# Kernel optimization log

Measured on AMD Instinct MI355X. Metric: run time of the kernel, lower is better.

## Reference

```python
import jax, jax.numpy as jnp
import numpy as np

T, N, D = 8, 50000, 128
H, M, E = 128, 64, 800000
TW = 10  # temporal conv kernel width


def setup_inputs() -> dict:
    key = jax.random.key(0)
    ks = jax.random.split(key, 16)
    s_d, s_2h, s_m, s_hm = D ** -0.5, (2 * H) ** -0.5, M ** -0.5, (H + M) ** -0.5
    return {
        "node_features": jax.random.normal(ks[0], (T, N, D), jnp.float32),
        "edge_index": jax.random.randint(ks[1], (2, E), 0, N, dtype=jnp.int64),
        # spatial dense [D -> H]
        "W_sp": jax.random.normal(ks[2], (D, H), jnp.float32) * s_d,
        "b_sp": jnp.zeros((H,), jnp.float32),
        # memory projection dense [2H -> M] (inline Dense, modeled shared)
        "W_mp": jax.random.normal(ks[3], (2 * H, M), jnp.float32) * s_2h,
        "b_mp": jnp.zeros((M,), jnp.float32),
        # flax GRUCell: input denses (ir,iz,in) with bias; hidden denses (hr,hz) no bias, hn with bias
        "Wi": jax.random.normal(ks[4], (M, 3 * M), jnp.float32) * s_m,
        "bi": jnp.zeros((3 * M,), jnp.float32),
        "Wh": jax.random.normal(ks[5], (M, 3 * M), jnp.float32) * s_m,
        "bhn": jnp.zeros((M,), jnp.float32),
        # output projection [H+M -> H]
        "W_out": jax.random.normal(ks[6], (H + M, H), jnp.float32) * s_hm,
        "b_out": jnp.zeros((H,), jnp.float32),
        # temporal conv kernel [TW, in=1, out=H] + bias [H] (only channel 0 is used)
        "conv_k": jax.random.normal(ks[7], (TW, 1, H), jnp.float32) * (TW ** -0.5),
        "conv_b": jnp.zeros((H,), jnp.float32),
    }


def _forward(node_features, edge_index, W_sp, b_sp, W_mp, b_mp, Wi, bi, Wh, bhn, W_out, b_out, conv_k, conv_b):
    t, n, _ = node_features.shape
    m = Wi.shape[0]
    src, tgt = edge_index[0], edge_index[1]

    def step(h, x_t):
        s = jax.nn.relu(x_t @ W_sp + b_sp)                       # [N,H]
        msg = jnp.zeros_like(s).at[tgt].add(s[src])               # scatter-add message passing
        mi = jnp.concatenate([s, msg], axis=-1) @ W_mp + b_mp     # [N,M]
        # flax GRUCell
        gi = mi @ Wi + bi                                         # [N,3M]
        gh = h @ Wh                                               # [N,3M] (no bias on hr/hz)
        i_r, i_z, i_n = jnp.split(gi, 3, axis=-1)
        h_r, h_z, h_n = jnp.split(gh, 3, axis=-1)
        r = jax.nn.sigmoid(i_r + h_r)
        z = jax.nn.sigmoid(i_z + h_z)
        nn_ = jnp.tanh(i_n + r * (h_n + bhn))
        h_new = (1.0 - z) * nn_ + z * h
        out = jnp.concatenate([s, h_new], axis=-1) @ W_out + b_out  # [N,H]
        return h_new, out

    h0 = jnp.zeros((n, m), node_features.dtype)
    h_final, outs = jax.lax.scan(step, h0, node_features)         # outs: [T,N,H]

    temporal = jnp.transpose(outs, (1, 0, 2))                     # [N,T,H]
    # flax Conv on [N,T,H,1]: batch=(N,T), spatial=H, in_ch=1; [...,0] keeps out channel 0
    x = temporal.reshape(n * t, -1, 1)                            # [N*T, H, 1]
    k0 = conv_k[:, :, :1]                                         # [TW,1,1]
    y = jax.lax.conv_general_dilated(x, k0, window_strides=(1,), padding="SAME",
                                     dimension_numbers=("NWC", "WIO", "NWC"))
    y = y[..., 0] + conv_b[0]                                     # [N*T, H]
    temporal_out = y.reshape(n, t, -1)                            # [N,T,H]
    final = temporal_out[:, -1, :]                                # [N,H]
    return final, h_final


def reference(node_features, edge_index, W_sp, b_sp, W_mp, b_mp, Wi, bi, Wh, bhn, W_out, b_out, conv_k, conv_b):
    return _forward(node_features, edge_index, W_sp, b_sp, W_mp, b_mp, Wi, bi, Wh, bhn, W_out, b_out, conv_k, conv_b)
```

## Files before the change

kernel.cpp:

```cpp
#include <hip/hip_runtime.h>

#define TT 8
#define NN 50000
#define DD 128
#define HH 128
#define MM 64
#define EE 800000
#define NBLK 196

typedef __attribute__((ext_vector_type(8))) short short8v;
typedef __attribute__((ext_vector_type(4))) float f32x4;

__device__ __forceinline__ short bf16rn(float v) {
    unsigned u = __builtin_bit_cast(unsigned, v);
    unsigned r = (u + 0x7fffu + ((u >> 16) & 1u)) >> 16;
    return (short)r;
}
__device__ __forceinline__ float bf16tof(short h) {
    unsigned u = ((unsigned)(unsigned short)h) << 16;
    return __builtin_bit_cast(float, u);
}
__device__ __forceinline__ void bsplit(float v, short& h, short& l) {
    h = bf16rn(v);
    l = bf16rn(v - bf16tof(h));
}
__device__ __forceinline__ f32x4 mfma16(short8v a, short8v b, f32x4 c) {
    return __builtin_amdgcn_mfma_f32_16x16x32_bf16(a, b, c, 0, 0, 0);
}

__global__ __launch_bounds__(256) void kConvEdges(const int* __restrict__ eraw,
                                                  int* __restrict__ src,
                                                  int* __restrict__ tgt,
                                                  int* __restrict__ deg) {
    bool is64 = true;
#pragma unroll
    for (int i = 0; i < 8; ++i)
        if (eraw[2 * i + 1] != 0) is64 = false;
    int i = blockIdx.x * blockDim.x + threadIdx.x;
    if (i < EE) {
        int s, t;
        if (is64) {
            const long long* e64 = (const long long*)eraw;
            s = (int)e64[i];
            t = (int)e64[EE + i];
        } else {
            s = eraw[i];
            t = eraw[EE + i];
        }
        s = min(max(s, 0), NN - 1);
        t = min(max(t, 0), NN - 1);
        src[i] = s;
        tgt[i] = t;
        atomicAdd(&deg[t], 1);
    }
}

__global__ __launch_bounds__(256) void kScanA(const int* __restrict__ deg,
                                              int* __restrict__ itmp,
                                              int* __restrict__ bsum) {
    __shared__ int sm[256];
    int gid = blockIdx.x * 256 + threadIdx.x;
    int v = (gid < NN) ? deg[gid] : 0;
    sm[threadIdx.x] = v;
    __syncthreads();
    for (int off = 1; off < 256; off <<= 1) {
        int add = (threadIdx.x >= off) ? sm[threadIdx.x - off] : 0;
        __syncthreads();
        sm[threadIdx.x] += add;
        __syncthreads();
    }
    itmp[gid] = sm[threadIdx.x];
    if (threadIdx.x == 255) bsum[blockIdx.x] = sm[255];
}

__global__ __launch_bounds__(256) void kScanB(const int* __restrict__ bsum,
                                              int* __restrict__ boffs) {
    __shared__ int sm[256];
    int v = (threadIdx.x < NBLK) ? bsum[threadIdx.x] : 0;
    sm[threadIdx.x] = v;
    __syncthreads();
    for (int off = 1; off < 256; off <<= 1) {
        int add = (threadIdx.x >= off) ? sm[threadIdx.x - off] : 0;
        __syncthreads();
        sm[threadIdx.x] += add;
        __syncthreads();
    }
    if (threadIdx.x < NBLK)
        boffs[threadIdx.x] = (threadIdx.x == 0) ? 0 : sm[threadIdx.x - 1];
}

__global__ __launch_bounds__(256) void kScanC(const int* __restrict__ itmp,
                                              const int* __restrict__ boffs,
                                              int* __restrict__ rowptr) {
    int gid = blockIdx.x * 256 + threadIdx.x;
    if (gid < NN) rowptr[gid + 1] = itmp[gid] + boffs[blockIdx.x];
    if (gid == 0) rowptr[0] = 0;
}

__global__ __launch_bounds__(256) void kFill(const int* __restrict__ src,
                                             const int* __restrict__ tgt,
                                             const int* __restrict__ rowptr,
                                             int* __restrict__ cursor,
                                             int* __restrict__ csr_src) {
    int e = blockIdx.x * blockDim.x + threadIdx.x;
    if (e < EE) {
        int t = tgt[e];
        int p = atomicAdd(&cursor[t], 1);
        csr_src[rowptr[t] + p] = src[e];
    }
}

__global__ __launch_bounds__(256) void kPrep(const float* __restrict__ Wsp,
                                             const float* __restrict__ Wmp,
                                             const float* __restrict__ bmp,
                                             const float* __restrict__ Wi,
                                             const float* __restrict__ bi,
                                             const float* __restrict__ Wh,
                                             const float* __restrict__ bhn,
                                             short* __restrict__ Bp1,
                                             short* __restrict__ Bp2,
                                             short* __restrict__ Bp3,
                                             float* __restrict__ bias_aq,
                                             float* __restrict__ bias_g) {
    const int gid = blockIdx.x * 256 + threadIdx.x;
    const int gstride = gridDim.x * 256;

    for (int i = gid; i < 8 * 4 * 512; i += gstride) {
        int e = i & 7, lanei = (i >> 3) & 63, kt = (i >> 9) & 3, nt = i >> 11;
        int k = kt * 32 + (lanei >> 4) * 8 + e;
        int col = nt * 16 + (lanei & 15);
        float v = Wsp[k * 128 + col];
        short h, l;
        bsplit(v, h, l);
        Bp1[((nt * 4 + kt) * 2 + 0) * 512 + lanei * 8 + e] = h;
        Bp1[((nt * 4 + kt) * 2 + 1) * 512 + lanei * 8 + e] = l;
    }
    for (int i = gid; i < 8 * 4 * 512; i += gstride) {
        int e = i & 7, lanei = (i >> 3) & 63, kt = (i >> 9) & 3, nt = i >> 11;
        int k = kt * 32 + (lanei >> 4) * 8 + e;
        int col = nt * 16 + (lanei & 15);
        float v = (col < 64) ? Wmp[k * 64 + col] : Wmp[(128 + k) * 64 + (col - 64)];
        short h, l;
        bsplit(v, h, l);
        Bp2[((nt * 4 + kt) * 2 + 0) * 512 + lanei * 8 + e] = h;
        Bp2[((nt * 4 + kt) * 2 + 1) * 512 + lanei * 8 + e] = l;
    }
    for (int i = gid; i < 16 * 4 * 512; i += gstride) {
        int e = i & 7, lanei = (i >> 3) & 63, kt = (i >> 9) & 3, nt = i >> 11;
        int k = kt * 32 + (lanei >> 4) * 8 + e;
        int col = nt * 16 + (lanei & 15);
        float v;
        if (k < 64) {
            v = (col < 192) ? Wi[k * 192 + col] : 0.f;
        } else {
            int kk = k - 64;
            if (col < 128)      v = Wh[kk * 192 + col];
            else if (col < 192) v = 0.f;
            else                v = Wh[kk * 192 + (col - 64)];
        }
        short h, l;
        bsplit(v, h, l);
        Bp3[((nt * 4 + kt) * 2 + 0) * 512 + lanei * 8 + e] = h;
        Bp3[((nt * 4 + kt) * 2 + 1) * 512 + lanei * 8 + e] = l;
    }
    if (gid < 128) bias_aq[gid] = (gid < 64) ? bmp[gid] : 0.f;
    if (gid < 256) bias_g[gid] = (gid < 192) ? bi[gid] : bhn[gid - 192];
}

__global__ __launch_bounds__(256) void kGemm12(const float* __restrict__ A,
                                               const short* __restrict__ Bp,
                                               const float* __restrict__ bias,
                                               float* __restrict__ C,
                                               int relu) {
    const int tid = threadIdx.x, lane = tid & 63, w = tid >> 6;
    const int rowBase = blockIdx.x * 64 + (w & 1) * 32;
    const int colBase = (w >> 1) * 64;

    short8v ah[2][4], al[2][4];
#pragma unroll
    for (int mt = 0; mt < 2; ++mt) {
        int row = min(rowBase + mt * 16 + (lane & 15), NN - 1);
        const float* ar = A + (size_t)row * 128 + (lane >> 4) * 8;
#pragma unroll
        for (int kt = 0; kt < 4; ++kt) {
            float4 x0 = *(const float4*)(ar + kt * 32);
            float4 x1 = *(const float4*)(ar + kt * 32 + 4);
            float xs[8] = {x0.x, x0.y, x0.z, x0.w, x1.x, x1.y, x1.z, x1.w};
#pragma unroll
            for (int e = 0; e < 8; ++e) {
                short h, l;
                bsplit(xs[e], h, l);
                ah[mt][kt][e] = h;
                al[mt][kt][e] = l;
            }
        }
    }

    f32x4 acc[2][4];
#pragma unroll
    for (int mt = 0; mt < 2; ++mt)
#pragma unroll
        for (int nt = 0; nt < 4; ++nt) acc[mt][nt] = (f32x4)0.f;

#pragma unroll
    for (int nt = 0; nt < 4; ++nt) {
        const int ntg = (colBase >> 4) + nt;
#pragma unroll
        for (int kt = 0; kt < 4; ++kt) {
            short8v bh = *(const short8v*)&Bp[((ntg * 4 + kt) * 2 + 0) * 512 + lane * 8];
            short8v bl = *(const short8v*)&Bp[((ntg * 4 + kt) * 2 + 1) * 512 + lane * 8];
#pragma unroll
            for (int mt = 0; mt < 2; ++mt) {
                acc[mt][nt] = mfma16(ah[mt][kt], bh, acc[mt][nt]);
                acc[mt][nt] = mfma16(ah[mt][kt], bl, acc[mt][nt]);
                acc[mt][nt] = mfma16(al[mt][kt], bh, acc[mt][nt]);
            }
        }
    }

#pragma unroll
    for (int mt = 0; mt < 2; ++mt)
#pragma unroll
        for (int nt = 0; nt < 4; ++nt) {
            int col = colBase + nt * 16 + (lane & 15);
            float bb = bias[col];
            int r0 = rowBase + mt * 16 + (lane >> 4) * 4;
#pragma unroll
            for (int r = 0; r < 4; ++r) {
                int row = r0 + r;
                if (row < NN) {
                    float v = acc[mt][nt][r] + bb;
                    if (relu) v = fmaxf(v, 0.f);
                    C[(size_t)row * 128 + col] = v;
                }
            }
        }
}

__global__ __launch_bounds__(256) void kGemm3(float* __restrict__ mih,
                                              const short* __restrict__ Bp,
                                              const float* __restrict__ bias_g) {
    __shared__ float gT[256][36];
    const int tid = threadIdx.x, lane = tid & 63, w = tid >> 6;
    const int rowBase = blockIdx.x * 32;
    const int colBase = w * 64;

    short8v ah[2][4], al[2][4];
#pragma unroll
    for (int mt = 0; mt < 2; ++mt) {
        int row = min(rowBase + mt * 16 + (lane & 15), NN - 1);
        const float* ar = mih + (size_t)row * 128 + (lane >> 4) * 8;
#pragma unroll
        for (int kt = 0; kt < 4; ++kt) {
            float4 x0 = *(const float4*)(ar + kt * 32);
            float4 x1 = *(const float4*)(ar + kt * 32 + 4);
            float xs[8] = {x0.x, x0.y, x0.z, x0.w, x1.x, x1.y, x1.z, x1.w};
#pragma unroll
            for (int e = 0; e < 8; ++e) {
                short h, l;
                bsplit(xs[e], h, l);
                ah[mt][kt][e] = h;
                al[mt][kt][e] = l;
            }
        }
    }

    f32x4 acc[2][4];
#pragma unroll
    for (int mt = 0; mt < 2; ++mt)
#pragma unroll
        for (int nt = 0; nt < 4; ++nt) acc[mt][nt] = (f32x4)0.f;

#pragma unroll
    for (int nt = 0; nt < 4; ++nt) {
        const int ntg = (colBase >> 4) + nt;
#pragma unroll
        for (int kt = 0; kt < 4; ++kt) {
            short8v bh = *(const short8v*)&Bp[((ntg * 4 + kt) * 2 + 0) * 512 + lane * 8];
            short8v bl = *(const short8v*)&Bp[((ntg * 4 + kt) * 2 + 1) * 512 + lane * 8];
#pragma unroll
            for (int mt = 0; mt < 2; ++mt) {
                acc[mt][nt] = mfma16(ah[mt][kt], bh, acc[mt][nt]);
                acc[mt][nt] = mfma16(ah[mt][kt], bl, acc[mt][nt]);
                acc[mt][nt] = mfma16(al[mt][kt], bh, acc[mt][nt]);
            }
        }
    }

#pragma unroll
    for (int mt = 0; mt < 2; ++mt)
#pragma unroll
        for (int nt = 0; nt < 4; ++nt) {
            int col = colBase + nt * 16 + (lane & 15);
            int r0 = mt * 16 + (lane >> 4) * 4;
            f32x4 v = acc[mt][nt] + bias_g[col];
            *(f32x4*)&gT[col][r0] = v;
        }
    __syncthreads();

#pragma unroll
    for (int i = 0; i < 8; ++i) {
        int idx = i * 256 + tid;
        int row = idx & 31, c = idx >> 5;
        int node = rowBase + row;
        if (node >= NN) continue;
        float xr = gT[c][row];
        float xz = gT[c + 64][row];
        float xni = gT[c + 128][row];
        float xnh = gT[c + 192][row];
        float* hp = &mih[(size_t)node * 128 + 64 + c];
        float hv = *hp;
        float r = 1.f / (1.f + __expf(-xr));
        float z = 1.f / (1.f + __expf(-xz));
        float xn = xni + r * xnh;
        float e2 = __expf(2.f * xn);
        float nn = 1.f - 2.f / (e2 + 1.f);
        *hp = (1.f - z) * nn + z * hv;
    }
}

__global__ __launch_bounds__(256) void kGather(const float* __restrict__ aq,
                                               const int* __restrict__ rowptr,
                                               const int* __restrict__ csr_src,
                                               float* __restrict__ mih) {
    const int lane = threadIdx.x & 63;
    const int w = (blockIdx.x * blockDim.x + threadIdx.x) >> 6;
    if (w >= NN) return;
    const int beg = rowptr[w];
    const int end = rowptr[w + 1];
    float acc0 = 0.f, acc1 = 0.f;
    int i = beg;
    for (; i + 1 < end; i += 2) {
        int s0 = csr_src[i];
        int s1 = csr_src[i + 1];
        acc0 += aq[(size_t)s0 * 128 + 64 + lane];
        acc1 += aq[(size_t)s1 * 128 + 64 + lane];
    }
    if (i < end) acc0 += aq[(size_t)csr_src[i] * 128 + 64 + lane];
    mih[(size_t)w * 128 + lane] = acc0 + acc1 + aq[(size_t)w * 128 + lane];
}

__global__ __launch_bounds__(128) void kD(const float* __restrict__ s_buf,
                                          const float* __restrict__ mih,
                                          const float* __restrict__ Wout,
                                          const float* __restrict__ bout,
                                          const float* __restrict__ convk,
                                          const float* __restrict__ convb,
                                          float* __restrict__ out) {
    __shared__ float ss[4][HH];
    __shared__ float hs[4][MM];
    __shared__ float os[4][HH];
    const int j = threadIdx.x;
    const int base = blockIdx.x * 4;

#pragma unroll
    for (int n = 0; n < 4; ++n)
        ss[n][j] = s_buf[(size_t)(base + n) * HH + j];
    for (int idx = j; idx < 4 * MM; idx += 128) {
        int n = idx >> 6, c = idx & 63;
        hs[n][c] = mih[(size_t)(base + n) * 128 + 64 + c];
    }
    __syncthreads();

    float acc[4];
    const float bj = bout[j];
#pragma unroll
    for (int n = 0; n < 4; ++n) acc[n] = bj;
#pragma unroll 4
    for (int k = 0; k < HH; ++k) {
        float w = Wout[k * HH + j];
#pragma unroll
        for (int n = 0; n < 4; ++n) acc[n] = fmaf(ss[n][k], w, acc[n]);
    }
#pragma unroll 4
    for (int k = 0; k < MM; ++k) {
        float w = Wout[(HH + k) * HH + j];
#pragma unroll
        for (int n = 0; n < 4; ++n) acc[n] = fmaf(hs[n][k], w, acc[n]);
    }
#pragma unroll
    for (int n = 0; n < 4; ++n) os[n][j] = acc[n];
    __syncthreads();

    float ck[10];
#pragma unroll
    for (int i = 0; i < 10; ++i) ck[i] = convk[i * HH];
    const float cb = convb[0];
#pragma unroll
    for (int n = 0; n < 4; ++n) {
        float y = cb;
#pragma unroll
        for (int i = 0; i < 10; ++i) {
            int p = j - 4 + i;
            float xv = (p >= 0 && p < HH) ? os[n][p] : 0.f;
            y = fmaf(xv, ck[i], y);
        }
        out[(size_t)(base + n) * HH + j] = y;
    }
    for (int idx = j; idx < 4 * MM; idx += 128) {
        int n = idx >> 6, c = idx & 63;
        out[(size_t)NN * HH + (size_t)(base + n) * MM + c] = hs[n][c];
    }
}

extern "C" void kernel_launch(void* const* d_in, const int* in_sizes, int n_in,
                              void* d_out, int out_size, void* d_ws, size_t ws_size,
                              hipStream_t stream) {
    const float* X    = (const float*)d_in[0];
    const int*   eraw = (const int*)d_in[1];
    const float* Wsp  = (const float*)d_in[2];
    const float* bsp  = (const float*)d_in[3];
    const float* Wmp  = (const float*)d_in[4];
    const float* bmp  = (const float*)d_in[5];
    const float* Wi   = (const float*)d_in[6];
    const float* bi   = (const float*)d_in[7];
    const float* Wh   = (const float*)d_in[8];
    const float* bhn  = (const float*)d_in[9];
    const float* Wout = (const float*)d_in[10];
    const float* bout = (const float*)d_in[11];
    const float* ck   = (const float*)d_in[12];
    const float* cb   = (const float*)d_in[13];
    float* out = (float*)d_out;

    float* ws = (float*)d_ws;
    float* s_buf  = ws;
    float* aq     = s_buf + (size_t)NN * 128;
    float* mih    = aq + (size_t)NN * 128;
    float* bias_aq= mih + (size_t)NN * 128;
    float* bias_g = bias_aq + 128;
    short* Bp1    = (short*)(bias_g + 256);
    short* Bp2    = Bp1 + 8 * 4 * 2 * 512;
    short* Bp3    = Bp2 + 8 * 4 * 2 * 512;
    int*   src     = (int*)(Bp3 + 16 * 4 * 2 * 512);
    int*   tgt     = src + EE;
    int*   csr_src = tgt + EE;
    int*   deg     = csr_src + EE;
    int*   rowptr  = deg + NN;
    int*   cursor  = rowptr + NN + 1;
    int*   itmp    = cursor + NN;
    int*   bsum    = itmp + NBLK * 256;
    int*   boffs   = bsum + 256;

    hipMemsetAsync(mih, 0, (size_t)NN * 128 * sizeof(float), stream);
    hipMemsetAsync(deg, 0, NN * sizeof(int), stream);
    hipMemsetAsync(cursor, 0, NN * sizeof(int), stream);

    kConvEdges<<<(EE + 255) / 256, 256, 0, stream>>>(eraw, src, tgt, deg);
    kScanA<<<NBLK, 256, 0, stream>>>(deg, itmp, bsum);
    kScanB<<<1, 256, 0, stream>>>(bsum, boffs);
    kScanC<<<NBLK, 256, 0, stream>>>(itmp, boffs, rowptr);
    kFill<<<(EE + 255) / 256, 256, 0, stream>>>(src, tgt, rowptr, cursor, csr_src);
    kPrep<<<64, 256, 0, stream>>>(Wsp, Wmp, bmp, Wi, bi, Wh, bhn,
                                  Bp1, Bp2, Bp3, bias_aq, bias_g);

    const int gx12 = (NN + 63) / 64;
    const int gx3  = (NN + 31) / 32;
    for (int t = 0; t < TT; ++t) {
        kGemm12<<<gx12, 256, 0, stream>>>(X + (size_t)t * NN * DD, Bp1, bsp, s_buf, 1);
        kGemm12<<<gx12, 256, 0, stream>>>(s_buf, Bp2, bias_aq, aq, 0);
        kGather<<<(NN * 64 + 255) / 256, 256, 0, stream>>>(aq, rowptr, csr_src, mih);
        kGemm3<<<gx3, 256, 0, stream>>>(mih, Bp3, bias_g);
    }
    kD<<<NN / 4, 128, 0, stream>>>(s_buf, mih, Wout, bout, ck, cb, out);
}
```

Baseline: 1.493 ms.

## Hoist feedforward GEMMs out of time loop and fuse into one batched kernel

The two non-recurrent GEMMs (spatial dense and the memory projection split into a/q halves) are computed for all T timesteps in a single fused kernel. The intermediate s stays in shared memory as packed hi/lo bf16 pairs, and only the last timestep's s is written out. The gathered neighbor projection q is stored as bf16 to halve gather traffic. The GRU input/state buffer is now kept as packed bf16 hi/lo words, so the per-element split no longer runs on load. This removes per-step launches and the round trip of s and aq through global memory, but adds larger a/q workspaces and reduces the precision of the message path and of the stored hidden state.

```diff
diff --git a/kernel.cpp b/kernel.cpp
--- a/kernel.cpp
+++ b/kernel.cpp
@@ -11,18 +11,28 @@
 typedef __attribute__((ext_vector_type(8))) short short8v;
 typedef __attribute__((ext_vector_type(4))) float f32x4;
 
-__device__ __forceinline__ short bf16rn(float v) {
+__device__ __forceinline__ unsigned bf16rn_bits(float v) {
     unsigned u = __builtin_bit_cast(unsigned, v);
-    unsigned r = (u + 0x7fffu + ((u >> 16) & 1u)) >> 16;
-    return (short)r;
-}
-__device__ __forceinline__ float bf16tof(short h) {
-    unsigned u = ((unsigned)(unsigned short)h) << 16;
-    return __builtin_bit_cast(float, u);
+    return (u + 0x7fffu + ((u >> 16) & 1u)) >> 16;
+}
+__device__ __forceinline__ short bf16rn(float v) { return (short)bf16rn_bits(v); }
+__device__ __forceinline__ float bf16tof_bits(unsigned hb16) {
+    return __builtin_bit_cast(float, hb16 << 16);
 }
 __device__ __forceinline__ void bsplit(float v, short& h, short& l) {
     h = bf16rn(v);
-    l = bf16rn(v - bf16tof(h));
+    l = bf16rn(v - bf16tof_bits((unsigned)(unsigned short)h));
+}
+__device__ __forceinline__ unsigned packsplit(float v) {
+    unsigned u = __builtin_bit_cast(unsigned, v);
+    unsigned hb = u & 0xFFFF0000u;
+    float lo = v - __builtin_bit_cast(float, hb);
+    return hb | (bf16rn_bits(lo) & 0xFFFFu);
+}
+__device__ __forceinline__ float unpack_val(unsigned p) {
+    float hi = __builtin_bit_cast(float, p & 0xFFFF0000u);
+    float lo = __builtin_bit_cast(float, p << 16);
+    return hi + lo;
 }
 __device__ __forceinline__ f32x4 mfma16(short8v a, short8v b, f32x4 c) {
     return __builtin_amdgcn_mfma_f32_16x16x32_bf16(a, b, c, 0, 0, 0);
@@ -112,7 +122,6 @@
 
 __global__ __launch_bounds__(256) void kPrep(const float* __restrict__ Wsp,
                                              const float* __restrict__ Wmp,
-                                             const float* __restrict__ bmp,
                                              const float* __restrict__ Wi,
                                              const float* __restrict__ bi,
                                              const float* __restrict__ Wh,
@@ -120,7 +129,6 @@
                                              short* __restrict__ Bp1,
                                              short* __restrict__ Bp2,
                                              short* __restrict__ Bp3,
-                                             float* __restrict__ bias_aq,
                                              float* __restrict__ bias_g) {
     const int gid = blockIdx.x * 256 + threadIdx.x;
     const int gstride = gridDim.x * 256;
@@ -163,24 +171,28 @@
         Bp3[((nt * 4 + kt) * 2 + 0) * 512 + lanei * 8 + e] = h;
         Bp3[((nt * 4 + kt) * 2 + 1) * 512 + lanei * 8 + e] = l;
     }
-    if (gid < 128) bias_aq[gid] = (gid < 64) ? bmp[gid] : 0.f;
     if (gid < 256) bias_g[gid] = (gid < 192) ? bi[gid] : bhn[gid - 192];
 }
 
-__global__ __launch_bounds__(256) void kGemm12(const float* __restrict__ A,
-                                               const short* __restrict__ Bp,
-                                               const float* __restrict__ bias,
-                                               float* __restrict__ C,
-                                               int relu) {
+__global__ __launch_bounds__(256) void kFF(const float* __restrict__ X,
+                                           const short* __restrict__ Bp1,
+                                           const float* __restrict__ bsp,
+                                           const short* __restrict__ Bp2,
+                                           const float* __restrict__ bmp,
+                                           float* __restrict__ a_all,
+                                           unsigned short* __restrict__ qb_all,
+                                           float* __restrict__ s_buf) {
+    __shared__ unsigned sPk[64][132];
     const int tid = threadIdx.x, lane = tid & 63, w = tid >> 6;
-    const int rowBase = blockIdx.x * 64 + (w & 1) * 32;
+    const size_t rowBlk = (size_t)blockIdx.x * 64;
+    const int rhalf = (w & 1) * 32;
     const int colBase = (w >> 1) * 64;
 
     short8v ah[2][4], al[2][4];
 #pragma unroll
     for (int mt = 0; mt < 2; ++mt) {
-        int row = min(rowBase + mt * 16 + (lane & 15), NN - 1);
-        const float* ar = A + (size_t)row * 128 + (lane >> 4) * 8;
+        size_t row = rowBlk + rhalf + mt * 16 + (lane & 15);
+        const float* ar = X + row * 128 + (lane >> 4) * 8;
 #pragma unroll
         for (int kt = 0; kt < 4; ++kt) {
             float4 x0 = *(const float4*)(ar + kt * 32);
@@ -207,8 +219,8 @@
         const int ntg = (colBase >> 4) + nt;
 #pragma unroll
         for (int kt = 0; kt < 4; ++kt) {
-            short8v bh = *(const short8v*)&Bp[((ntg * 4 + kt) * 2 + 0) * 512 + lane * 8];
-            short8v bl = *(const short8v*)&Bp[((ntg * 4 + kt) * 2 + 1) * 512 + lane * 8];
+            short8v bh = *(const short8v*)&Bp1[((ntg * 4 + kt) * 2 + 0) * 512 + lane * 8];
+            short8v bl = *(const short8v*)&Bp1[((ntg * 4 + kt) * 2 + 1) * 512 + lane * 8];
 #pragma unroll
             for (int mt = 0; mt < 2; ++mt) {
                 acc[mt][nt] = mfma16(ah[mt][kt], bh, acc[mt][nt]);
@@ -223,49 +235,36 @@
 #pragma unroll
         for (int nt = 0; nt < 4; ++nt) {
             int col = colBase + nt * 16 + (lane & 15);
-            float bb = bias[col];
-            int r0 = rowBase + mt * 16 + (lane >> 4) * 4;
+            float b = bsp[col];
+            int lr0 = rhalf + mt * 16 + (lane >> 4) * 4;
 #pragma unroll
             for (int r = 0; r < 4; ++r) {
-                int row = r0 + r;
-                if (row < NN) {
-                    float v = acc[mt][nt][r] + bb;
-                    if (relu) v = fmaxf(v, 0.f);
-                    C[(size_t)row * 128 + col] = v;
-                }
-            }
-        }
-}
-
-__global__ __launch_bounds__(256) void kGemm3(float* __restrict__ mih,
-                                              const short* __restrict__ Bp,
-                                              const float* __restrict__ bias_g) {
-    __shared__ float gT[256][36];
-    const int tid = threadIdx.x, lane = tid & 63, w = tid >> 6;
-    const int rowBase = blockIdx.x * 32;
-    const int colBase = w * 64;
-
-    short8v ah[2][4], al[2][4];
+                float sv = fmaxf(acc[mt][nt][r] + b, 0.f);
+                sPk[lr0 + r][col] = packsplit(sv);
+                size_t row = rowBlk + lr0 + r;
+                if (row >= (size_t)(TT - 1) * NN)
+                    s_buf[(row - (size_t)(TT - 1) * NN) * 128 + col] = sv;
+            }
+        }
+    __syncthreads();
+
 #pragma unroll
     for (int mt = 0; mt < 2; ++mt) {
-        int row = min(rowBase + mt * 16 + (lane & 15), NN - 1);
-        const float* ar = mih + (size_t)row * 128 + (lane >> 4) * 8;
+        int lr = rhalf + mt * 16 + (lane & 15);
 #pragma unroll
         for (int kt = 0; kt < 4; ++kt) {
-            float4 x0 = *(const float4*)(ar + kt * 32);
-            float4 x1 = *(const float4*)(ar + kt * 32 + 4);
-            float xs[8] = {x0.x, x0.y, x0.z, x0.w, x1.x, x1.y, x1.z, x1.w};
+            int k0 = kt * 32 + (lane >> 4) * 8;
+            uint4 p0 = *(const uint4*)&sPk[lr][k0];
+            uint4 p1 = *(const uint4*)&sPk[lr][k0 + 4];
+            unsigned ps[8] = {p0.x, p0.y, p0.z, p0.w, p1.x, p1.y, p1.z, p1.w};
 #pragma unroll
             for (int e = 0; e < 8; ++e) {
-                short h, l;
-                bsplit(xs[e], h, l);
-                ah[mt][kt][e] = h;
-                al[mt][kt][e] = l;
-            }
-        }
-    }
-
-    f32x4 acc[2][4];
+                ah[mt][kt][e] = (short)(ps[e] >> 16);
+                al[mt][kt][e] = (short)(ps[e] & 0xFFFFu);
+            }
+        }
+    }
+
 #pragma unroll
     for (int mt = 0; mt < 2; ++mt)
 #pragma unroll
@@ -276,8 +275,8 @@
         const int ntg = (colBase >> 4) + nt;
 #pragma unroll
         for (int kt = 0; kt < 4; ++kt) {
-            short8v bh = *(const short8v*)&Bp[((ntg * 4 + kt) * 2 + 0) * 512 + lane * 8];
-            short8v bl = *(const short8v*)&Bp[((ntg * 4 + kt) * 2 + 1) * 512 + lane * 8];
+            short8v bh = *(const short8v*)&Bp2[((ntg * 4 + kt) * 2 + 0) * 512 + lane * 8];
+            short8v bl = *(const short8v*)&Bp2[((ntg * 4 + kt) * 2 + 1) * 512 + lane * 8];
 #pragma unroll
             for (int mt = 0; mt < 2; ++mt) {
                 acc[mt][nt] = mfma16(ah[mt][kt], bh, acc[mt][nt]);
@@ -292,37 +291,30 @@
 #pragma unroll
         for (int nt = 0; nt < 4; ++nt) {
             int col = colBase + nt * 16 + (lane & 15);
-            int r0 = mt * 16 + (lane >> 4) * 4;
-            f32x4 v = acc[mt][nt] + bias_g[col];
-            *(f32x4*)&gT[col][r0] = v;
-        }
-    __syncthreads();
-
-#pragma unroll
-    for (int i = 0; i < 8; ++i) {
-        int idx = i * 256 + tid;
-        int row = idx & 31, c = idx >> 5;
-        int node = rowBase + row;
-        if (node >= NN) continue;
-        float xr = gT[c][row];
-        float xz = gT[c + 64][row];
-        float xni = gT[c + 128][row];
-        float xnh = gT[c + 192][row];
-        float* hp = &mih[(size_t)node * 128 + 64 + c];
-        float hv = *hp;
-        float r = 1.f / (1.f + __expf(-xr));
-        float z = 1.f / (1.f + __expf(-xz));
-        float xn = xni + r * xnh;
-        float e2 = __expf(2.f * xn);
-        float nn = 1.f - 2.f / (e2 + 1.f);
-        *hp = (1.f - z) * nn + z * hv;
-    }
-}
-
-__global__ __launch_bounds__(256) void kGather(const float* __restrict__ aq,
-                                               const int* __restrict__ rowptr,
-                                               const int* __restrict__ csr_src,
-                                               float* __restrict__ mih) {
+            int lr0 = rhalf + mt * 16 + (lane >> 4) * 4;
+            if (col < 64) {
+                float b = bmp[col];
+#pragma unroll
+                for (int r = 0; r < 4; ++r) {
+                    size_t row = rowBlk + lr0 + r;
+                    a_all[row * 64 + col] = acc[mt][nt][r] + b;
+                }
+            } else {
+#pragma unroll
+                for (int r = 0; r < 4; ++r) {
+                    size_t row = rowBlk + lr0 + r;
+                    qb_all[row * 64 + (col - 64)] =
+                        (unsigned short)bf16rn_bits(acc[mt][nt][r]);
+                }
+            }
+        }
+}
+
+__global__ __launch_bounds__(256) void kGatherB(const float* __restrict__ a_t,
+                                                const unsigned short* __restrict__ qb_t,
+                                                const int* __restrict__ rowptr,
+                                                const int* __restrict__ csr_src,
+                                                unsigned* __restrict__ mihp) {
     const int lane = threadIdx.x & 63;
     const int w = (blockIdx.x * blockDim.x + threadIdx.x) >> 6;
     if (w >= NN) return;
@@ -333,15 +325,96 @@
     for (; i + 1 < end; i += 2) {
         int s0 = csr_src[i];
         int s1 = csr_src[i + 1];
-        acc0 += aq[(size_t)s0 * 128 + 64 + lane];
-        acc1 += aq[(size_t)s1 * 128 + 64 + lane];
-    }
-    if (i < end) acc0 += aq[(size_t)csr_src[i] * 128 + 64 + lane];
-    mih[(size_t)w * 128 + lane] = acc0 + acc1 + aq[(size_t)w * 128 + lane];
+        acc0 += bf16tof_bits(qb_t[(size_t)s0 * 64 + lane]);
+        acc1 += bf16tof_bits(qb_t[(size_t)s1 * 64 + lane]);
+    }
+    if (i < end) acc0 += bf16tof_bits(qb_t[(size_t)csr_src[i] * 64 + lane]);
+    float mi = acc0 + acc1 + a_t[(size_t)w * 64 + lane];
+    mihp[(size_t)w * 128 + lane] = packsplit(mi);
+}
+
+__global__ __launch_bounds__(256) void kGemm3(unsigned* __restrict__ mihp,
+                                              const short* __restrict__ Bp3,
+                                              const float* __restrict__ bias_g) {
+    __shared__ float gT[256][36];
+    const int tid = threadIdx.x, lane = tid & 63, w = tid >> 6;
+    const int rowBase = blockIdx.x * 32;
+    const int colBase = w * 64;
+
+    short8v ah[2][4], al[2][4];
+#pragma unroll
+    for (int mt = 0; mt < 2; ++mt) {
+        int row = min(rowBase + mt * 16 + (lane & 15), NN - 1);
+        const unsigned* ar = mihp + (size_t)row * 128 + (lane >> 4) * 8;
+#pragma unroll
+        for (int kt = 0; kt < 4; ++kt) {
+            uint4 p0 = *(const uint4*)(ar + kt * 32);
+            uint4 p1 = *(const uint4*)(ar + kt * 32 + 4);
+            unsigned ps[8] = {p0.x, p0.y, p0.z, p0.w, p1.x, p1.y, p1.z, p1.w};
+#pragma unroll
+            for (int e = 0; e < 8; ++e) {
+                ah[mt][kt][e] = (short)(ps[e] >> 16);
+                al[mt][kt][e] = (short)(ps[e] & 0xFFFFu);
+            }
+        }
+    }
+
+    f32x4 acc[2][4];
+#pragma unroll
+    for (int mt = 0; mt < 2; ++mt)
+#pragma unroll
+        for (int nt = 0; nt < 4; ++nt) acc[mt][nt] = (f32x4)0.f;
+
+#pragma unroll
+    for (int nt = 0; nt < 4; ++nt) {
+        const int ntg = (colBase >> 4) + nt;
+#pragma unroll
+        for (int kt = 0; kt < 4; ++kt) {
+            short8v bh = *(const short8v*)&Bp3[((ntg * 4 + kt) * 2 + 0) * 512 + lane * 8];
+            short8v bl = *(const short8v*)&Bp3[((ntg * 4 + kt) * 2 + 1) * 512 + lane * 8];
+#pragma unroll
+            for (int mt = 0; mt < 2; ++mt) {
+                acc[mt][nt] = mfma16(ah[mt][kt], bh, acc[mt][nt]);
+                acc[mt][nt] = mfma16(ah[mt][kt], bl, acc[mt][nt]);
+                acc[mt][nt] = mfma16(al[mt][kt], bh, acc[mt][nt]);
+            }
+        }
+    }
+
+#pragma unroll
+    for (int mt = 0; mt < 2; ++mt)
+#pragma unroll
+        for (int nt = 0; nt < 4; ++nt) {
+            int col = colBase + nt * 16 + (lane & 15);
+            int r0 = mt * 16 + (lane >> 4) * 4;
+            f32x4 v = acc[mt][nt] + bias_g[col];
+            *(f32x4*)&gT[col][r0] = v;
+        }
+    __syncthreads();
+
+#pragma unroll
+    for (int i = 0; i < 8; ++i) {
+        int idx = i * 256 + tid;
+        int row = idx & 31, c = idx >> 5;
+        int node = rowBase + row;
+        if (node >= NN) continue;
+        float xr = gT[c][row];
+        float xz = gT[c + 64][row];
+        float xni = gT[c + 128][row];
+        float xnh = gT[c + 192][row];
+        unsigned* hp = &mihp[(size_t)node * 128 + 64 + c];
+        float hv = unpack_val(*hp);
+        float r = 1.f / (1.f + __expf(-xr));
+        float z = 1.f / (1.f + __expf(-xz));
+        float xn = xni + r * xnh;
+        float e2 = __expf(2.f * xn);
+        float nn = 1.f - 2.f / (e2 + 1.f);
+        *hp = packsplit((1.f - z) * nn + z * hv);
+    }
 }
 
 __global__ __launch_bounds__(128) void kD(const float* __restrict__ s_buf,
-                                          const float* __restrict__ mih,
+                                          const unsigned* __restrict__ mihp,
                                           const float* __restrict__ Wout,
                                           const float* __restrict__ bout,
                                           const float* __restrict__ convk,
@@ -358,7 +431,7 @@
         ss[n][j] = s_buf[(size_t)(base + n) * HH + j];
     for (int idx = j; idx < 4 * MM; idx += 128) {
         int n = idx >> 6, c = idx & 63;
-        hs[n][c] = mih[(size_t)(base + n) * 128 + 64 + c];
+        hs[n][c] = unpack_val(mihp[(size_t)(base + n) * 128 + 64 + c]);
     }
     __syncthreads();
 
@@ -423,25 +496,25 @@
     float* out = (float*)d_out;
 
     float* ws = (float*)d_ws;
-    float* s_buf  = ws;
-    float* aq     = s_buf + (size_t)NN * 128;
-    float* mih    = aq + (size_t)NN * 128;
-    float* bias_aq= mih + (size_t)NN * 128;
-    float* bias_g = bias_aq + 128;
-    short* Bp1    = (short*)(bias_g + 256);
-    short* Bp2    = Bp1 + 8 * 4 * 2 * 512;
-    short* Bp3    = Bp2 + 8 * 4 * 2 * 512;
-    int*   src     = (int*)(Bp3 + 16 * 4 * 2 * 512);
-    int*   tgt     = src + EE;
-    int*   csr_src = tgt + EE;
-    int*   deg     = csr_src + EE;
-    int*   rowptr  = deg + NN;
-    int*   cursor  = rowptr + NN + 1;
-    int*   itmp    = cursor + NN;
-    int*   bsum    = itmp + NBLK * 256;
-    int*   boffs   = bsum + 256;
-
-    hipMemsetAsync(mih, 0, (size_t)NN * 128 * sizeof(float), stream);
+    float*    s_buf  = ws;
+    float*    a_all  = s_buf + (size_t)NN * 128;
+    unsigned short* qb_all = (unsigned short*)(a_all + (size_t)TT * NN * 64);
+    unsigned* mihp   = (unsigned*)(qb_all + (size_t)TT * NN * 64);
+    float*    bias_g = (float*)(mihp + (size_t)NN * 128);
+    short*    Bp1    = (short*)(bias_g + 256);
+    short*    Bp2    = Bp1 + 8 * 4 * 2 * 512;
+    short*    Bp3    = Bp2 + 8 * 4 * 2 * 512;
+    int*      src     = (int*)(Bp3 + 16 * 4 * 2 * 512);
+    int*      tgt     = src + EE;
+    int*      csr_src = tgt + EE;
+    int*      deg     = csr_src + EE;
+    int*      rowptr  = deg + NN;
+    int*      cursor  = rowptr + NN + 1;
+    int*      itmp    = cursor + NN;
+    int*      bsum    = itmp + NBLK * 256;
+    int*      boffs   = bsum + 256;
+
+    hipMemsetAsync(mihp, 0, (size_t)NN * 128 * sizeof(unsigned), stream);
     hipMemsetAsync(deg, 0, NN * sizeof(int), stream);
     hipMemsetAsync(cursor, 0, NN * sizeof(int), stream);
 
@@ -450,16 +523,16 @@
     kScanB<<<1, 256, 0, stream>>>(bsum, boffs);
     kScanC<<<NBLK, 256, 0, stream>>>(itmp, boffs, rowptr);
     kFill<<<(EE + 255) / 256, 256, 0, stream>>>(src, tgt, rowptr, cursor, csr_src);
-    kPrep<<<64, 256, 0, stream>>>(Wsp, Wmp, bmp, Wi, bi, Wh, bhn,
-                                  Bp1, Bp2, Bp3, bias_aq, bias_g);
-
-    const int gx12 = (NN + 63) / 64;
-    const int gx3  = (NN + 31) / 32;
+    kPrep<<<64, 256, 0, stream>>>(Wsp, Wmp, Wi, bi, Wh, bhn, Bp1, Bp2, Bp3, bias_g);
+
+    kFF<<<(TT * NN) / 64, 256, 0, stream>>>(X, Bp1, bsp, Bp2, bmp, a_all, qb_all, s_buf);
+
+    const int gx3 = (NN + 31) / 32;
     for (int t = 0; t < TT; ++t) {
-        kGemm12<<<gx12, 256, 0, stream>>>(X + (size_t)t * NN * DD, Bp1, bsp, s_buf, 1);
-        kGemm12<<<gx12, 256, 0, stream>>>(s_buf, Bp2, bias_aq, aq, 0);
-        kGather<<<(NN * 64 + 255) / 256, 256, 0, stream>>>(aq, rowptr, csr_src, mih);
-        kGemm3<<<gx3, 256, 0, stream>>>(mih, Bp3, bias_g);
-    }
-    kD<<<NN / 4, 128, 0, stream>>>(s_buf, mih, Wout, bout, ck, cb, out);
-}
+        kGatherB<<<(NN * 64 + 255) / 256, 256, 0, stream>>>(
+            a_all + (size_t)t * NN * 64, qb_all + (size_t)t * NN * 64,
+            rowptr, csr_src, mihp);
+        kGemm3<<<gx3, 256, 0, stream>>>(mihp, Bp3, bias_g);
+    }
+    kD<<<NN / 4, 128, 0, stream>>>(s_buf, mihp, Wout, bout, ck, cb, out);
+}
```

New measurement: 1.281 ms. 1.17x faster.
